# Kernel optimization log

Measured on AMD Instinct MI355X. Metric: run time of the kernel, lower is better.

The kernel has to match this reference:

```python
import math
import jax, jax.numpy as jnp
import numpy as np

NUM_HEADS = 8
ALPHA = 20.0
LN_EPS = 1e-5


def setup_inputs() -> dict:
    key = jax.random.key(0)
    ks = jax.random.split(key, 6)
    B, N, C = 8, 4096, 512
    s = 1.0 / math.sqrt(C)
    return {
        "x": jax.random.normal(ks[0], (B, N, C), dtype=jnp.float32),
        "qkv_w": jax.random.normal(ks[1], (C, 3 * C), dtype=jnp.float32) * s,
        "qkv_b": jnp.zeros((3 * C,), dtype=jnp.float32),
        "ln_g": jnp.ones((C,), dtype=jnp.float32),
        "ln_b": jnp.zeros((C,), dtype=jnp.float32),
        "out_w": jax.random.normal(ks[2], (C, C), dtype=jnp.float32) * s,
        "out_b": jnp.zeros((C,), dtype=jnp.float32),
    }


def _forward(x, qkv_w, qkv_b, ln_g, ln_b, out_w, out_b):
    B, N, C = x.shape
    H = NUM_HEADS
    D = C // H
    qkv = x @ qkv_w + qkv_b  # (B,N,3C)
    q, k, v = jnp.split(qkv, 3, axis=-1)

    def to_heads(t):
        return t.reshape(B, N, H, D).transpose(0, 2, 1, 3)  # (B,H,N,D)

    q, k, v = to_heads(q), to_heads(k), to_heads(v)

    # cosine-inhibit feature maps
    q_norm = jnp.linalg.norm(q, axis=-1, keepdims=True)  # (B,H,N,1)
    k_norm = jnp.linalg.norm(k, axis=-1, keepdims=True)
    q_t = q / q_norm
    dq = jnp.tanh(q / q_norm * ALPHA) * (math.pi / 4)
    dk = jnp.tanh(k / k_norm * ALPHA) * (math.pi / 4)
    k3 = jnp.abs(k) ** 3
    kf = jnp.concatenate([k3 * jnp.cos(dk), k3 * jnp.sin(dk)], axis=-1)  # (B,H,N,2D)
    power = 1.5 * (0.5 + jnp.tanh(q_norm))
    q_t = (q_t ** 2) ** power
    qf = jnp.concatenate([q_t * jnp.cos(dq), q_t * jnp.sin(dq)], axis=-1)  # (B,H,N,2D)

    # O(N) linear attention
    k_mean = jnp.mean(kf, axis=2, keepdims=True)  # (B,H,1,2D)
    z = 1.0 / (jnp.einsum('bhnf,bhmf->bhnm', qf, k_mean) + 1e-6)  # (B,H,N,1)
    scale = N ** (-0.5)
    kv = jnp.einsum('bhnf,bhnd->bhfd', kf * scale, v * scale)  # (B,H,2D,D)
    out = jnp.einsum('bhnf,bhfd->bhnd', qf, kv) * z  # (B,H,N,D)

    out = out.transpose(0, 2, 1, 3).reshape(B, N, C)
    # LayerNorm
    mu = jnp.mean(out, axis=-1, keepdims=True)
    var = jnp.var(out, axis=-1, keepdims=True)
    out = (out - mu) * jax.lax.rsqrt(var + LN_EPS) * ln_g + ln_b
    return out @ out_w + out_b


def reference(x, qkv_w, qkv_b, ln_g, ln_b, out_w, out_b):
    return _forward(x, qkv_w, qkv_b, ln_g, ln_b, out_w, out_b)
```

## Files before the change

kernel.cpp:

```cpp
#include <hip/hip_runtime.h>
#include <math.h>

#define Bb 8
#define Nn 4096
#define Cc 512
#define Hh 8
#define Dd 64
#define Ff 128
#define M_ROWS (Bb * Nn)
#define PI4f 0.78539816339744830962f
#define CHB 16
#define PART 8320

using bf16x8 = __attribute__((ext_vector_type(8))) short;
using f32x4 = __attribute__((ext_vector_type(4))) float;

__device__ __forceinline__ unsigned short f2bf(float f) {
  unsigned u = __float_as_uint(f);
  u += 0x7FFFu + ((u >> 16) & 1u);
  return (unsigned short)(u >> 16);
}
__device__ __forceinline__ float bf2f(unsigned short h) {
  return __uint_as_float(((unsigned)h) << 16);
}
__device__ __forceinline__ float grp16_sum(float v) {
  v += __shfl_xor(v, 1);
  v += __shfl_xor(v, 2);
  v += __shfl_xor(v, 4);
  v += __shfl_xor(v, 8);
  return v;
}
__device__ __forceinline__ float wsum64(float v) {
#pragma unroll
  for (int m = 32; m >= 1; m >>= 1) v += __shfl_xor(v, m, 64);
  return v;
}

__global__ __launch_bounds__(256) void x_convert(const float* __restrict__ x,
                                                 unsigned short* __restrict__ xb) {
  size_t i = ((size_t)blockIdx.x * 256 + threadIdx.x) * 8;
  float4 a = *(const float4*)(x + i);
  float4 b = *(const float4*)(x + i + 4);
  int4 o;
  o.x = (int)f2bf(a.x) | ((int)f2bf(a.y) << 16);
  o.y = (int)f2bf(a.z) | ((int)f2bf(a.w) << 16);
  o.z = (int)f2bf(b.x) | ((int)f2bf(b.y) << 16);
  o.w = (int)f2bf(b.z) | ((int)f2bf(b.w) << 16);
  *(int4*)(xb + i) = o;
}

__global__ __launch_bounds__(256) void w_transpose(const float* __restrict__ qkvw,
                                                   const float* __restrict__ outw,
                                                   unsigned short* __restrict__ wt,
                                                   unsigned short* __restrict__ owt) {
  __shared__ float tile[64][65];
  const int bid = blockIdx.x;
  const float* src;
  unsigned short* dst;
  int ldsrc, j0, k0;
  if (bid < 192) {
    src = qkvw; dst = wt; ldsrc = 1536;
    j0 = (bid % 24) * 64; k0 = (bid / 24) * 64;
  } else {
    int r = bid - 192;
    src = outw; dst = owt; ldsrc = 512;
    j0 = (r & 7) * 64; k0 = (r >> 3) * 64;
  }
  const int t = threadIdx.x;
  const int rr = t >> 4, cc = (t & 15) * 4;
#pragma unroll
  for (int it = 0; it < 4; ++it) {
    float4 v = *(const float4*)(src + (size_t)(k0 + rr + it * 16) * ldsrc + j0 + cc);
    tile[rr + it * 16][cc + 0] = v.x;
    tile[rr + it * 16][cc + 1] = v.y;
    tile[rr + it * 16][cc + 2] = v.z;
    tile[rr + it * 16][cc + 3] = v.w;
  }
  __syncthreads();
  const int j = t >> 2, kq = (t & 3) * 16;
  unsigned short u[16];
#pragma unroll
  for (int p = 0; p < 16; ++p) u[p] = f2bf(tile[kq + p][j]);
  int4 o;
  o.x = (int)u[0] | ((int)u[1] << 16);
  o.y = (int)u[2] | ((int)u[3] << 16);
  o.z = (int)u[4] | ((int)u[5] << 16);
  o.w = (int)u[6] | ((int)u[7] << 16);
  int4 o2;
  o2.x = (int)u[8] | ((int)u[9] << 16);
  o2.y = (int)u[10] | ((int)u[11] << 16);
  o2.z = (int)u[12] | ((int)u[13] << 16);
  o2.w = (int)u[14] | ((int)u[15] << 16);
  *(int4*)(dst + (size_t)(j0 + j) * 512 + k0 + kq) = o;
  *(int4*)(dst + (size_t)(j0 + j) * 512 + k0 + kq + 8) = o2;
}

__global__ __launch_bounds__(256) void kv_kernel(const unsigned short* __restrict__ xb,
                                                 const unsigned short* __restrict__ wt,
                                                 const float* __restrict__ qkvb,
                                                 float* __restrict__ part) {
  __shared__ char smraw[53248];
  unsigned short* As = (unsigned short*)smraw;
  unsigned short* Bs = As + 128 * 72;
  unsigned short* kf_t = (unsigned short*)smraw;
  unsigned short* v_t = kf_t + 128 * 136;
  float* ksl = (float*)(smraw + 52224);
  const int t = threadIdx.x, lane = t & 63, wv = t >> 6;
  const int i = lane & 15, g = lane >> 4, kq = g * 8;
  const int wm = wv >> 1, wn = wv & 1;
  const int bh = blockIdx.x >> 4, chunk = blockIdx.x & 15;
  const int b = bh >> 3, h = bh & 7;
  const int sr = t >> 1, sko = (t & 1) * 32;
  const int wrow = (sr < 64) ? (512 + h * 64 + sr) : (1024 + h * 64 + sr - 64);
  const unsigned short* bg = wt + (size_t)wrow * 512 + sko;
  float bias_[4];
  const int cb = ((wn == 0) ? 512 : 1024) + h * 64 + i;
#pragma unroll
  for (int ni = 0; ni < 4; ++ni) bias_[ni] = qkvb[cb + 16 * ni];
  f32x4 kvf[4][2] = {};
  float ksc[4] = {0.f, 0.f, 0.f, 0.f}, kss[4] = {0.f, 0.f, 0.f, 0.f};

  for (int t2 = 0; t2 < 2; ++t2) {
    const size_t row0 = (size_t)b * Nn + chunk * 256 + t2 * 128;
    const unsigned short* ag = xb + (row0 + sr) * 512 + sko;
    bf16x8 pa[4], pb[4];
#pragma unroll
    for (int p = 0; p < 4; ++p) {
      pa[p] = *(const bf16x8*)(ag + p * 8);
      pb[p] = *(const bf16x8*)(bg + p * 8);
    }
    f32x4 acc[4][4] = {};
    for (int k0 = 0; k0 < 512; k0 += 64) {
      __syncthreads();
#pragma unroll
      for (int p = 0; p < 4; ++p) {
        *(bf16x8*)&As[sr * 72 + sko + p * 8] = pa[p];
        *(bf16x8*)&Bs[sr * 72 + sko + p * 8] = pb[p];
      }
      __syncthreads();
      if (k0 < 448) {
#pragma unroll
        for (int p = 0; p < 4; ++p) {
          pa[p] = *(const bf16x8*)(ag + k0 + 64 + p * 8);
          pb[p] = *(const bf16x8*)(bg + k0 + 64 + p * 8);
        }
      }
#pragma unroll
      for (int ks = 0; ks < 2; ++ks) {
        bf16x8 am[4], bn[4];
#pragma unroll
        for (int q = 0; q < 4; ++q) {
          am[q] = *(const bf16x8*)&As[(64 * wm + 16 * q + i) * 72 + ks * 32 + kq];
          bn[q] = *(const bf16x8*)&Bs[(64 * wn + 16 * q + i) * 72 + ks * 32 + kq];
        }
#pragma unroll
        for (int mi = 0; mi < 4; ++mi)
#pragma unroll
          for (int ni = 0; ni < 4; ++ni)
            acc[mi][ni] = __builtin_amdgcn_mfma_f32_16x16x32_bf16(am[mi], bn[ni], acc[mi][ni], 0, 0, 0);
      }
    }
    __syncthreads();
    if (wn == 0) {
#pragma unroll
      for (int mi = 0; mi < 4; ++mi) {
        float nrm[4];
#pragma unroll
        for (int r = 0; r < 4; ++r) {
          float s = 0.f;
#pragma unroll
          for (int ni = 0; ni < 4; ++ni) {
            float kx = acc[mi][ni][r] + bias_[ni];
            s += kx * kx;
          }
          nrm[r] = sqrtf(grp16_sum(s));
        }
#pragma unroll
        for (int ni = 0; ni < 4; ++ni)
#pragma unroll
          for (int r = 0; r < 4; ++r) {
            float kx = acc[mi][ni][r] + bias_[ni];
            float dk = tanhf(kx / nrm[r] * 20.0f) * PI4f;
            float a3 = fabsf(kx);
            a3 = a3 * a3 * a3;
            float sn, cs;
            __sincosf(dk, &sn, &cs);
            float kc = a3 * cs, ksn = a3 * sn;
            ksc[ni] += kc;
            kss[ni] += ksn;
            const int nl = 64 * wm + 16 * mi + 4 * g + r;
            kf_t[(16 * ni + i) * 136 + nl] = f2bf(kc);
            kf_t[(64 + 16 * ni + i) * 136 + nl] = f2bf(ksn);
          }
      }
    } else {
#pragma unroll
      for (int mi = 0; mi < 4; ++mi)
#pragma unroll
        for (int ni = 0; ni < 4; ++ni)
#pragma unroll
          for (int r = 0; r < 4; ++r) {
            const int nl = 64 * wm + 16 * mi + 4 * g + r;
            v_t[(16 * ni + i) * 136 + nl] = f2bf(acc[mi][ni][r] + bias_[ni]);
          }
    }
    __syncthreads();
#pragma unroll
    for (int ks2 = 0; ks2 < 4; ++ks2) {
      bf16x8 a2[4], b2[2];
#pragma unroll
      for (int mi = 0; mi < 4; ++mi)
        a2[mi] = *(const bf16x8*)&kf_t[(64 * wm + 16 * mi + i) * 136 + ks2 * 32 + kq];
#pragma unroll
      for (int ni = 0; ni < 2; ++ni)
        b2[ni] = *(const bf16x8*)&v_t[(32 * wn + 16 * ni + i) * 136 + ks2 * 32 + kq];
#pragma unroll
      for (int mi = 0; mi < 4; ++mi)
#pragma unroll
        for (int ni = 0; ni < 2; ++ni)
          kvf[mi][ni] = __builtin_amdgcn_mfma_f32_16x16x32_bf16(a2[mi], b2[ni], kvf[mi][ni], 0, 0, 0);
    }
  }
  float* pw = part + (size_t)blockIdx.x * PART;
#pragma unroll
  for (int mi = 0; mi < 4; ++mi)
#pragma unroll
    for (int ni = 0; ni < 2; ++ni)
#pragma unroll
      for (int r = 0; r < 4; ++r)
        pw[(64 * wm + 16 * mi + 4 * g + r) * 64 + 32 * wn + 16 * ni + i] = kvf[mi][ni][r];
  if (wn == 0) {
#pragma unroll
    for (int ni = 0; ni < 4; ++ni) {
      float c = ksc[ni];
      c += __shfl_xor(c, 16);
      c += __shfl_xor(c, 32);
      float s = kss[ni];
      s += __shfl_xor(s, 16);
      s += __shfl_xor(s, 32);
      if (lane < 16) {
        ksl[wm * 128 + 16 * ni + lane] = c;
        ksl[wm * 128 + 64 + 16 * ni + lane] = s;
      }
    }
  }
  __syncthreads();
  if (t < 128) pw[8192 + t] = ksl[t] + ksl[128 + t];
}

__global__ __launch_bounds__(256) void kv_reduce(const float* __restrict__ part,
                                                 unsigned short* __restrict__ kvt,
                                                 float* __restrict__ kmean) {
  const int bh = blockIdx.x;
  const float invN = 1.0f / Nn;
  const size_t base = (size_t)bh * CHB * PART;
  for (int idx = threadIdx.x; idx < 8192; idx += 256) {
    float s = 0.f;
#pragma unroll
    for (int c = 0; c < CHB; ++c) s += part[base + (size_t)c * PART + idx];
    int f = idx >> 6, d = idx & 63;
    kvt[(size_t)bh * 8192 + d * 128 + f] = f2bf(s * invN);
  }
  if (threadIdx.x < 128) {
    float s = 0.f;
#pragma unroll
    for (int c = 0; c < CHB; ++c) s += part[base + (size_t)c * PART + 8192 + threadIdx.x];
    kmean[bh * 128 + threadIdx.x] = s * invN;
  }
}

__global__ __launch_bounds__(256) void attn_kernel(const unsigned short* __restrict__ xb,
                                                   const unsigned short* __restrict__ wt,
                                                   const float* __restrict__ qkvb,
                                                   const unsigned short* __restrict__ kvt,
                                                   const float* __restrict__ kmean,
                                                   unsigned short* __restrict__ attb) {
  __shared__ char smraw[52736];
  unsigned short* As = (unsigned short*)smraw;
  unsigned short* Bs = As + 128 * 72;
  unsigned short* qf_t = (unsigned short*)smraw;
  unsigned short* kv_s = (unsigned short*)(smraw + 34816);
  float* km = (float*)(smraw + 34816 + 17408);
  const int t = threadIdx.x, lane = t & 63, wv = t >> 6;
  const int i = lane & 15, g = lane >> 4, kq = g * 8;
  const int bh = blockIdx.x >> 5, chunk = blockIdx.x & 31;
  const int b = bh >> 3, h = bh & 7;
  const size_t row0 = (size_t)b * Nn + chunk * 128;
  if (t < 128) km[t] = kmean[bh * 128 + t];
  {
    const unsigned short* src = kvt + (size_t)bh * 8192;
#pragma unroll
    for (int it = 0; it < 4; ++it) {
      int idx = t + it * 256;
      int d = idx >> 4, f8 = (idx & 15) * 8;
      *(bf16x8*)&kv_s[d * 136 + f8] = *(const bf16x8*)(src + d * 128 + f8);
    }
  }
  const int sr = t >> 1, sko = (t & 1) * 32;
  const int c2 = t >> 2, ko2 = (t & 3) * 16;
  const unsigned short* ag = xb + (row0 + sr) * 512 + sko;
  const unsigned short* bgq = wt + (size_t)(h * 64 + c2) * 512 + ko2;
  bf16x8 pa[4], pb[2];
#pragma unroll
  for (int p = 0; p < 4; ++p) pa[p] = *(const bf16x8*)(ag + p * 8);
#pragma unroll
  for (int p = 0; p < 2; ++p) pb[p] = *(const bf16x8*)(bgq + p * 8);
  f32x4 acc[2][4] = {};
  for (int k0 = 0; k0 < 512; k0 += 64) {
    __syncthreads();
#pragma unroll
    for (int p = 0; p < 4; ++p) *(bf16x8*)&As[sr * 72 + sko + p * 8] = pa[p];
#pragma unroll
    for (int p = 0; p < 2; ++p) *(bf16x8*)&Bs[c2 * 72 + ko2 + p * 8] = pb[p];
    __syncthreads();
    if (k0 < 448) {
#pragma unroll
      for (int p = 0; p < 4; ++p) pa[p] = *(const bf16x8*)(ag + k0 + 64 + p * 8);
#pragma unroll
      for (int p = 0; p < 2; ++p) pb[p] = *(const bf16x8*)(bgq + k0 + 64 + p * 8);
    }
#pragma unroll
    for (int ks = 0; ks < 2; ++ks) {
      bf16x8 am[2], bn[4];
#pragma unroll
      for (int mi = 0; mi < 2; ++mi)
        am[mi] = *(const bf16x8*)&As[(32 * wv + 16 * mi + i) * 72 + ks * 32 + kq];
#pragma unroll
      for (int ni = 0; ni < 4; ++ni)
        bn[ni] = *(const bf16x8*)&Bs[(16 * ni + i) * 72 + ks * 32 + kq];
#pragma unroll
      for (int mi = 0; mi < 2; ++mi)
#pragma unroll
        for (int ni = 0; ni < 4; ++ni)
          acc[mi][ni] = __builtin_amdgcn_mfma_f32_16x16x32_bf16(am[mi], bn[ni], acc[mi][ni], 0, 0, 0);
    }
  }
  __syncthreads();
  float bqv[4];
#pragma unroll
  for (int ni = 0; ni < 4; ++ni) bqv[ni] = qkvb[h * 64 + 16 * ni + i];
  float z[2][4];
#pragma unroll
  for (int mi = 0; mi < 2; ++mi) {
    float nrm[4];
#pragma unroll
    for (int r = 0; r < 4; ++r) {
      float s = 0.f;
#pragma unroll
      for (int ni = 0; ni < 4; ++ni) {
        float q = acc[mi][ni][r] + bqv[ni];
        s += q * q;
      }
      nrm[r] = sqrtf(grp16_sum(s));
    }
#pragma unroll
    for (int r = 0; r < 4; ++r) {
      float pwr = 1.5f * (0.5f + tanhf(nrm[r]));
      float dp = 0.f;
      const int nl = 32 * wv + 16 * mi + 4 * g + r;
#pragma unroll
      for (int ni = 0; ni < 4; ++ni) {
        float q = acc[mi][ni][r] + bqv[ni];
        float qt = q / nrm[r];
        float dq = tanhf(qt * 20.0f) * PI4f;
        float qtp = exp2f(pwr * __log2f(qt * qt));
        float sn, cs;
        __sincosf(dq, &sn, &cs);
        float qc = qtp * cs, qs = qtp * sn;
        dp += qc * km[16 * ni + i] + qs * km[64 + 16 * ni + i];
        qf_t[nl * 136 + 16 * ni + i] = f2bf(qc);
        qf_t[nl * 136 + 64 + 16 * ni + i] = f2bf(qs);
      }
      z[mi][r] = 1.0f / (grp16_sum(dp) + 1e-6f);
    }
  }
  __syncthreads();
  f32x4 pacc[2][4] = {};
#pragma unroll
  for (int ks2 = 0; ks2 < 4; ++ks2) {
    bf16x8 a2[2], b2[4];
#pragma unroll
    for (int mi = 0; mi < 2; ++mi)
      a2[mi] = *(const bf16x8*)&qf_t[(32 * wv + 16 * mi + i) * 136 + ks2 * 32 + kq];
#pragma unroll
    for (int ni = 0; ni < 4; ++ni)
      b2[ni] = *(const bf16x8*)&kv_s[(16 * ni + i) * 136 + ks2 * 32 + kq];
#pragma unroll
    for (int mi = 0; mi < 2; ++mi)
#pragma unroll
      for (int ni = 0; ni < 4; ++ni)
        pacc[mi][ni] = __builtin_amdgcn_mfma_f32_16x16x32_bf16(a2[mi], b2[ni], pacc[mi][ni], 0, 0, 0);
  }
#pragma unroll
  for (int mi = 0; mi < 2; ++mi)
#pragma unroll
    for (int ni = 0; ni < 4; ++ni)
#pragma unroll
      for (int r = 0; r < 4; ++r)
        attb[(row0 + 32 * wv + 16 * mi + 4 * g + r) * 512 + h * 64 + 16 * ni + i] =
            f2bf(pacc[mi][ni][r] * z[mi][r]);
}

__global__ __launch_bounds__(256) void ln_kernel(unsigned short* __restrict__ attb,
                                                 const float* __restrict__ gg,
                                                 const float* __restrict__ bb) {
  const int lane = threadIdx.x & 63, wv = threadIdx.x >> 6;
  const size_t row = (size_t)blockIdx.x * 4 + wv;
  unsigned short* p = attb + row * 512 + lane * 8;
  bf16x8 v = *(bf16x8*)p;
  float x[8];
#pragma unroll
  for (int j = 0; j < 8; ++j) x[j] = bf2f((unsigned short)v[j]);
  float s = 0.f;
#pragma unroll
  for (int j = 0; j < 8; ++j) s += x[j];
  const float mu = wsum64(s) * (1.0f / 512.0f);
  float sq = 0.f;
#pragma unroll
  for (int j = 0; j < 8; ++j) {
    float d = x[j] - mu;
    sq += d * d;
  }
  const float rstd = rsqrtf(wsum64(sq) * (1.0f / 512.0f) + 1e-5f);
  const float4 g0 = *(const float4*)(gg + lane * 8);
  const float4 g1 = *(const float4*)(gg + lane * 8 + 4);
  const float4 b0 = *(const float4*)(bb + lane * 8);
  const float4 b1 = *(const float4*)(bb + lane * 8 + 4);
  float gv[8] = {g0.x, g0.y, g0.z, g0.w, g1.x, g1.y, g1.z, g1.w};
  float bv[8] = {b0.x, b0.y, b0.z, b0.w, b1.x, b1.y, b1.z, b1.w};
#pragma unroll
  for (int j = 0; j < 8; ++j)
    v[j] = (short)f2bf((x[j] - mu) * rstd * gv[j] + bv[j]);
  *(bf16x8*)p = v;
}

__global__ __launch_bounds__(256) void out_gemm(const unsigned short* __restrict__ attb,
                                                const unsigned short* __restrict__ owt,
                                                const float* __restrict__ ob,
                                                float* __restrict__ outp) {
  __shared__ unsigned short As[128 * 72];
  __shared__ unsigned short Bs[128 * 72];
  const int t = threadIdx.x, lane = t & 63, wv = t >> 6;
  const int i = lane & 15, g = lane >> 4, kq = g * 8;
  const int wm = wv >> 1, wn = wv & 1;
  const int m0 = (blockIdx.x >> 2) * 128, n0 = (blockIdx.x & 3) * 128;
  const int sr = t >> 1, sko = (t & 1) * 32;
  const unsigned short* ag = attb + (size_t)(m0 + sr) * 512 + sko;
  const unsigned short* bg = owt + (size_t)(n0 + sr) * 512 + sko;
  f32x4 acc[4][4] = {};
  bf16x8 pa[4], pb[4];
#pragma unroll
  for (int p = 0; p < 4; ++p) {
    pa[p] = *(const bf16x8*)(ag + p * 8);
    pb[p] = *(const bf16x8*)(bg + p * 8);
  }
  for (int k0 = 0; k0 < 512; k0 += 64) {
    __syncthreads();
#pragma unroll
    for (int p = 0; p < 4; ++p) {
      *(bf16x8*)&As[sr * 72 + sko + p * 8] = pa[p];
      *(bf16x8*)&Bs[sr * 72 + sko + p * 8] = pb[p];
    }
    __syncthreads();
    if (k0 < 448) {
#pragma unroll
      for (int p = 0; p < 4; ++p) {
        pa[p] = *(const bf16x8*)(ag + k0 + 64 + p * 8);
        pb[p] = *(const bf16x8*)(bg + k0 + 64 + p * 8);
      }
    }
#pragma unroll
    for (int ks = 0; ks < 2; ++ks) {
      bf16x8 am[4], bn[4];
#pragma unroll
      for (int q = 0; q < 4; ++q) {
        am[q] = *(const bf16x8*)&As[(64 * wm + 16 * q + i) * 72 + ks * 32 + kq];
        bn[q] = *(const bf16x8*)&Bs[(64 * wn + 16 * q + i) * 72 + ks * 32 + kq];
      }
#pragma unroll
      for (int mi = 0; mi < 4; ++mi)
#pragma unroll
        for (int ni = 0; ni < 4; ++ni)
          acc[mi][ni] = __builtin_amdgcn_mfma_f32_16x16x32_bf16(am[mi], bn[ni], acc[mi][ni], 0, 0, 0);
    }
  }
#pragma unroll
  for (int ni = 0; ni < 4; ++ni) {
    float bv = ob[n0 + 64 * wn + 16 * ni + i];
#pragma unroll
    for (int mi = 0; mi < 4; ++mi)
#pragma unroll
      for (int r = 0; r < 4; ++r)
        outp[(size_t)(m0 + 64 * wm + 16 * mi + 4 * g + r) * 512 + n0 + 64 * wn +
             16 * ni + i] = acc[mi][ni][r] + bv;
  }
}

extern "C" void kernel_launch(void* const* d_in, const int* in_sizes, int n_in,
                              void* d_out, int out_size, void* d_ws,
                              size_t ws_size, hipStream_t stream) {
  const float* x = (const float*)d_in[0];
  const float* qkv_w = (const float*)d_in[1];
  const float* qkv_b = (const float*)d_in[2];
  const float* ln_g = (const float*)d_in[3];
  const float* ln_b = (const float*)d_in[4];
  const float* out_w = (const float*)d_in[5];
  const float* out_b = (const float*)d_in[6];
  float* out = (float*)d_out;

  char* w = (char*)d_ws;
  unsigned short* xb = (unsigned short*)w;
  unsigned short* wt = (unsigned short*)(w + 33554432);
  unsigned short* owt = (unsigned short*)(w + 35127296);
  unsigned short* kvt = (unsigned short*)(w + 35651584);
  float* kmean = (float*)(w + 36700160);
  char* R = w + 36732928;
  float* part = (float*)R;
  unsigned short* attb = (unsigned short*)R;

  x_convert<<<8192, 256, 0, stream>>>(x, xb);
  w_transpose<<<256, 256, 0, stream>>>(qkv_w, out_w, wt, owt);
  kv_kernel<<<1024, 256, 0, stream>>>(xb, wt, qkv_b, part);
  kv_reduce<<<64, 256, 0, stream>>>(part, kvt, kmean);
  attn_kernel<<<2048, 256, 0, stream>>>(xb, wt, qkv_b, kvt, kmean, attb);
  ln_kernel<<<8192, 256, 0, stream>>>(attb, ln_g, ln_b);
  out_gemm<<<1024, 256, 0, stream>>>(attb, owt, out_b, out);
}
```

Measured before the change: 399.5 us.

## Rebalance kv_kernel warps across rows, use fast tanh, prefetch next tile

kv_kernel changes its warp split from a 2x2 grid, where only half the warps ran the costly K feature map, to each warp owning 32 rows across all 128 K and V columns. Every warp now shares the tanh/sincos work and the K-sum reduction. The first tile of the second row block is prefetched during the last k-step of the first. tanhf is replaced with an exp-based fast_tanh in both kernels, which is cheaper but may overflow to inf/NaN-safe edge cases and is slightly less accurate.

```diff
diff --git a/kernel.cpp b/kernel.cpp
--- a/kernel.cpp
+++ b/kernel.cpp
@@ -34,6 +34,10 @@
 #pragma unroll
   for (int m = 32; m >= 1; m >>= 1) v += __shfl_xor(v, m, 64);
   return v;
+}
+__device__ __forceinline__ float fast_tanh(float x) {
+  float e = __expf(2.0f * x);
+  return 1.0f - 2.0f / (e + 1.0f);
 }
 
 __global__ __launch_bounds__(256) void x_convert(const float* __restrict__ x,
@@ -99,7 +103,7 @@
                                                  const unsigned short* __restrict__ wt,
                                                  const float* __restrict__ qkvb,
                                                  float* __restrict__ part) {
-  __shared__ char smraw[53248];
+  __shared__ char smraw[54272];
   unsigned short* As = (unsigned short*)smraw;
   unsigned short* Bs = As + 128 * 72;
   unsigned short* kf_t = (unsigned short*)smraw;
@@ -107,29 +111,29 @@
   float* ksl = (float*)(smraw + 52224);
   const int t = threadIdx.x, lane = t & 63, wv = t >> 6;
   const int i = lane & 15, g = lane >> 4, kq = g * 8;
-  const int wm = wv >> 1, wn = wv & 1;
   const int bh = blockIdx.x >> 4, chunk = blockIdx.x & 15;
   const int b = bh >> 3, h = bh & 7;
   const int sr = t >> 1, sko = (t & 1) * 32;
   const int wrow = (sr < 64) ? (512 + h * 64 + sr) : (1024 + h * 64 + sr - 64);
   const unsigned short* bg = wt + (size_t)wrow * 512 + sko;
-  float bias_[4];
-  const int cb = ((wn == 0) ? 512 : 1024) + h * 64 + i;
-#pragma unroll
-  for (int ni = 0; ni < 4; ++ni) bias_[ni] = qkvb[cb + 16 * ni];
-  f32x4 kvf[4][2] = {};
+  float bias_[8];
+#pragma unroll
+  for (int ni = 0; ni < 4; ++ni) bias_[ni] = qkvb[512 + h * 64 + 16 * ni + i];
+#pragma unroll
+  for (int ni = 4; ni < 8; ++ni) bias_[ni] = qkvb[1024 + h * 64 + 16 * (ni - 4) + i];
+  f32x4 kvf[2][4] = {};
   float ksc[4] = {0.f, 0.f, 0.f, 0.f}, kss[4] = {0.f, 0.f, 0.f, 0.f};
-
+  const size_t rowbase = (size_t)b * Nn + chunk * 256;
+  const unsigned short* ag0 = xb + (rowbase + sr) * 512 + sko;
+  bf16x8 pa[4], pb[4];
+#pragma unroll
+  for (int p = 0; p < 4; ++p) {
+    pa[p] = *(const bf16x8*)(ag0 + p * 8);
+    pb[p] = *(const bf16x8*)(bg + p * 8);
+  }
   for (int t2 = 0; t2 < 2; ++t2) {
-    const size_t row0 = (size_t)b * Nn + chunk * 256 + t2 * 128;
-    const unsigned short* ag = xb + (row0 + sr) * 512 + sko;
-    bf16x8 pa[4], pb[4];
-#pragma unroll
-    for (int p = 0; p < 4; ++p) {
-      pa[p] = *(const bf16x8*)(ag + p * 8);
-      pb[p] = *(const bf16x8*)(bg + p * 8);
-    }
-    f32x4 acc[4][4] = {};
+    const unsigned short* ag = xb + (rowbase + t2 * 128 + sr) * 512 + sko;
+    f32x4 acc[2][8] = {};
     for (int k0 = 0; k0 < 512; k0 += 64) {
       __syncthreads();
 #pragma unroll
@@ -144,108 +148,109 @@
           pa[p] = *(const bf16x8*)(ag + k0 + 64 + p * 8);
           pb[p] = *(const bf16x8*)(bg + k0 + 64 + p * 8);
         }
+      } else if (t2 == 0) {
+        const unsigned short* ag1 = ag + 128 * 512;
+#pragma unroll
+        for (int p = 0; p < 4; ++p) {
+          pa[p] = *(const bf16x8*)(ag1 + p * 8);
+          pb[p] = *(const bf16x8*)(bg + p * 8);
+        }
       }
 #pragma unroll
       for (int ks = 0; ks < 2; ++ks) {
-        bf16x8 am[4], bn[4];
-#pragma unroll
-        for (int q = 0; q < 4; ++q) {
-          am[q] = *(const bf16x8*)&As[(64 * wm + 16 * q + i) * 72 + ks * 32 + kq];
-          bn[q] = *(const bf16x8*)&Bs[(64 * wn + 16 * q + i) * 72 + ks * 32 + kq];
+        bf16x8 am[2], bn[8];
+#pragma unroll
+        for (int mi = 0; mi < 2; ++mi)
+          am[mi] = *(const bf16x8*)&As[(32 * wv + 16 * mi + i) * 72 + ks * 32 + kq];
+#pragma unroll
+        for (int ni = 0; ni < 8; ++ni)
+          bn[ni] = *(const bf16x8*)&Bs[(16 * ni + i) * 72 + ks * 32 + kq];
+#pragma unroll
+        for (int mi = 0; mi < 2; ++mi)
+#pragma unroll
+          for (int ni = 0; ni < 8; ++ni)
+            acc[mi][ni] = __builtin_amdgcn_mfma_f32_16x16x32_bf16(am[mi], bn[ni], acc[mi][ni], 0, 0, 0);
+      }
+    }
+    __syncthreads();
+#pragma unroll
+    for (int mi = 0; mi < 2; ++mi) {
+      float nrm[4];
+#pragma unroll
+      for (int r = 0; r < 4; ++r) {
+        float s = 0.f;
+#pragma unroll
+        for (int ni = 0; ni < 4; ++ni) {
+          float kx = acc[mi][ni][r] + bias_[ni];
+          s += kx * kx;
         }
-#pragma unroll
-        for (int mi = 0; mi < 4; ++mi)
-#pragma unroll
-          for (int ni = 0; ni < 4; ++ni)
-            acc[mi][ni] = __builtin_amdgcn_mfma_f32_16x16x32_bf16(am[mi], bn[ni], acc[mi][ni], 0, 0, 0);
-      }
+        nrm[r] = sqrtf(grp16_sum(s));
+      }
+#pragma unroll
+      for (int ni = 0; ni < 4; ++ni)
+#pragma unroll
+        for (int r = 0; r < 4; ++r) {
+          float kx = acc[mi][ni][r] + bias_[ni];
+          float dk = fast_tanh(kx / nrm[r] * 20.0f) * PI4f;
+          float a3 = fabsf(kx);
+          a3 = a3 * a3 * a3;
+          float sn, cs;
+          __sincosf(dk, &sn, &cs);
+          float kc = a3 * cs, ksn = a3 * sn;
+          ksc[ni] += kc;
+          kss[ni] += ksn;
+          const int nl = 32 * wv + 16 * mi + 4 * g + r;
+          kf_t[(16 * ni + i) * 136 + nl] = f2bf(kc);
+          kf_t[(64 + 16 * ni + i) * 136 + nl] = f2bf(ksn);
+        }
+#pragma unroll
+      for (int ni = 4; ni < 8; ++ni)
+#pragma unroll
+        for (int r = 0; r < 4; ++r) {
+          const int nl = 32 * wv + 16 * mi + 4 * g + r;
+          v_t[(16 * (ni - 4) + i) * 136 + nl] = f2bf(acc[mi][ni][r] + bias_[ni]);
+        }
     }
     __syncthreads();
-    if (wn == 0) {
-#pragma unroll
-      for (int mi = 0; mi < 4; ++mi) {
-        float nrm[4];
-#pragma unroll
-        for (int r = 0; r < 4; ++r) {
-          float s = 0.f;
-#pragma unroll
-          for (int ni = 0; ni < 4; ++ni) {
-            float kx = acc[mi][ni][r] + bias_[ni];
-            s += kx * kx;
-          }
-          nrm[r] = sqrtf(grp16_sum(s));
-        }
+#pragma unroll
+    for (int ks2 = 0; ks2 < 4; ++ks2) {
+      bf16x8 a2[2], b2[4];
+#pragma unroll
+      for (int mi = 0; mi < 2; ++mi)
+        a2[mi] = *(const bf16x8*)&kf_t[(32 * wv + 16 * mi + i) * 136 + ks2 * 32 + kq];
+#pragma unroll
+      for (int ni = 0; ni < 4; ++ni)
+        b2[ni] = *(const bf16x8*)&v_t[(16 * ni + i) * 136 + ks2 * 32 + kq];
+#pragma unroll
+      for (int mi = 0; mi < 2; ++mi)
 #pragma unroll
         for (int ni = 0; ni < 4; ++ni)
-#pragma unroll
-          for (int r = 0; r < 4; ++r) {
-            float kx = acc[mi][ni][r] + bias_[ni];
-            float dk = tanhf(kx / nrm[r] * 20.0f) * PI4f;
-            float a3 = fabsf(kx);
-            a3 = a3 * a3 * a3;
-            float sn, cs;
-            __sincosf(dk, &sn, &cs);
-            float kc = a3 * cs, ksn = a3 * sn;
-            ksc[ni] += kc;
-            kss[ni] += ksn;
-            const int nl = 64 * wm + 16 * mi + 4 * g + r;
-            kf_t[(16 * ni + i) * 136 + nl] = f2bf(kc);
-            kf_t[(64 + 16 * ni + i) * 136 + nl] = f2bf(ksn);
-          }
-      }
-    } else {
-#pragma unroll
-      for (int mi = 0; mi < 4; ++mi)
-#pragma unroll
-        for (int ni = 0; ni < 4; ++ni)
-#pragma unroll
-          for (int r = 0; r < 4; ++r) {
-            const int nl = 64 * wm + 16 * mi + 4 * g + r;
-            v_t[(16 * ni + i) * 136 + nl] = f2bf(acc[mi][ni][r] + bias_[ni]);
-          }
-    }
-    __syncthreads();
-#pragma unroll
-    for (int ks2 = 0; ks2 < 4; ++ks2) {
-      bf16x8 a2[4], b2[2];
-#pragma unroll
-      for (int mi = 0; mi < 4; ++mi)
-        a2[mi] = *(const bf16x8*)&kf_t[(64 * wm + 16 * mi + i) * 136 + ks2 * 32 + kq];
-#pragma unroll
-      for (int ni = 0; ni < 2; ++ni)
-        b2[ni] = *(const bf16x8*)&v_t[(32 * wn + 16 * ni + i) * 136 + ks2 * 32 + kq];
-#pragma unroll
-      for (int mi = 0; mi < 4; ++mi)
-#pragma unroll
-        for (int ni = 0; ni < 2; ++ni)
           kvf[mi][ni] = __builtin_amdgcn_mfma_f32_16x16x32_bf16(a2[mi], b2[ni], kvf[mi][ni], 0, 0, 0);
     }
   }
   float* pw = part + (size_t)blockIdx.x * PART;
 #pragma unroll
-  for (int mi = 0; mi < 4; ++mi)
-#pragma unroll
-    for (int ni = 0; ni < 2; ++ni)
+  for (int mi = 0; mi < 2; ++mi)
+#pragma unroll
+    for (int ni = 0; ni < 4; ++ni)
 #pragma unroll
       for (int r = 0; r < 4; ++r)
-        pw[(64 * wm + 16 * mi + 4 * g + r) * 64 + 32 * wn + 16 * ni + i] = kvf[mi][ni][r];
-  if (wn == 0) {
-#pragma unroll
-    for (int ni = 0; ni < 4; ++ni) {
-      float c = ksc[ni];
-      c += __shfl_xor(c, 16);
-      c += __shfl_xor(c, 32);
-      float s = kss[ni];
-      s += __shfl_xor(s, 16);
-      s += __shfl_xor(s, 32);
-      if (lane < 16) {
-        ksl[wm * 128 + 16 * ni + lane] = c;
-        ksl[wm * 128 + 64 + 16 * ni + lane] = s;
-      }
+        pw[(32 * wv + 16 * mi + 4 * g + r) * 64 + 16 * ni + i] = kvf[mi][ni][r];
+#pragma unroll
+  for (int ni = 0; ni < 4; ++ni) {
+    float c = ksc[ni];
+    c += __shfl_xor(c, 16);
+    c += __shfl_xor(c, 32);
+    float s = kss[ni];
+    s += __shfl_xor(s, 16);
+    s += __shfl_xor(s, 32);
+    if (lane < 16) {
+      ksl[wv * 128 + 16 * ni + lane] = c;
+      ksl[wv * 128 + 64 + 16 * ni + lane] = s;
     }
   }
   __syncthreads();
-  if (t < 128) pw[8192 + t] = ksl[t] + ksl[128 + t];
+  if (t < 128) pw[8192 + t] = ksl[t] + ksl[128 + t] + ksl[256 + t] + ksl[384 + t];
 }
 
 __global__ __launch_bounds__(256) void kv_reduce(const float* __restrict__ part,
@@ -355,14 +360,14 @@
     }
 #pragma unroll
     for (int r = 0; r < 4; ++r) {
-      float pwr = 1.5f * (0.5f + tanhf(nrm[r]));
+      float pwr = 1.5f * (0.5f + fast_tanh(nrm[r]));
       float dp = 0.f;
       const int nl = 32 * wv + 16 * mi + 4 * g + r;
 #pragma unroll
       for (int ni = 0; ni < 4; ++ni) {
         float q = acc[mi][ni][r] + bqv[ni];
         float qt = q / nrm[r];
-        float dq = tanhf(qt * 20.0f) * PI4f;
+        float dq = fast_tanh(qt * 20.0f) * PI4f;
         float qtp = exp2f(pwr * __log2f(qt * qt));
         float sn, cs;
         __sincosf(dq, &sn, &cs);
```

Result: faster. 357.8 us (-10.4%).
